# Kernel tuning notes

Measured on AMD Instinct MI355X. Metric: run time of the kernel, lower is better.

Reference implementation:

```python
import jax, jax.numpy as jnp
import numpy as np

B, K, E, D = 256, 2, 16, 512  # batch, top_k, num_experts, input_dim==output_dim
EPS = 1e-5  # nn.LayerNorm default eps
SCALE = 0.02  # param init scale


def setup_inputs() -> dict:
    key = jax.random.key(0)
    ks = jax.random.split(key, 9)
    return {
        "x": jax.random.normal(ks[0], (B, D), dtype=jnp.float32),
        "weight_probs": jax.random.uniform(ks[1], (B, K), dtype=jnp.float32),
        "bias_probs": jax.random.uniform(ks[2], (B, K), dtype=jnp.float32),
        "input_weight_bank": jax.random.normal(ks[3], (E, D, D), dtype=jnp.float32) * SCALE,
        "output_weight_bank": jax.random.normal(ks[4], (E, D, D), dtype=jnp.float32) * SCALE,
        "diagonal_weight_bank": jax.random.normal(ks[5], (E, D, D), dtype=jnp.float32) * SCALE,
        "bias_bank": jax.random.normal(ks[6], (E, D, D), dtype=jnp.float32) * SCALE,
        "weight_indices": jax.random.randint(ks[7], (B, K), 0, E),
        "bias_indices": jax.random.randint(ks[8], (B, K), 0, E),
    }


def reference(x, weight_probs, bias_probs, input_weight_bank, output_weight_bank,
              diagonal_weight_bank, bias_bank, weight_indices, bias_indices):
    # gather per-example expert parameter slabs: [B, K, D, D]
    iv = jnp.einsum('bi,bkij->bkj', x, input_weight_bank[weight_indices])     # [B,K,D]
    ov = jnp.einsum('bi,bkij->bkj', x, output_weight_bank[weight_indices])    # [B,K,D]
    dv = jnp.einsum('bi,bkij->bkj', x, diagonal_weight_bank[weight_indices])  # [B,K,D]

    # outer-product generated weight matrix + dynamic diagonal (in==out, no padding)
    outer = iv[..., :, None] * ov[..., None, :]                               # [B,K,D,D]
    r = jnp.arange(D)
    W = outer.at[..., r, r].add(dv)                                           # add diag embed

    # probability-weighted combine over top-k (weight_probs reshaped (-1,K,1,1) in torch)
    Wmix = jnp.einsum('bk,bkio->bio', weight_probs, W)                        # [B,D,D]

    # LayerNorm over output_dim, elementwise_affine=False
    mu = jnp.mean(Wmix, axis=-1, keepdims=True)
    var = jnp.var(Wmix, axis=-1, keepdims=True)
    Wn = (Wmix - mu) * jax.lax.rsqrt(var + EPS)

    # generated biases: gather + einsum + weighted combine ((-1,K,1) reshape)
    bv = jnp.einsum('bi,bkio->bko', x, bias_bank[bias_indices])               # [B,K,D]
    bmix = jnp.einsum('bk,bko->bo', bias_probs, bv)                           # [B,D]
    return (Wn, bmix)
```

## Files before the change

kernel.cpp:

```cpp
#include <hip/hip_runtime.h>
#include <math.h>

#define BB 256
#define KK 2
#define EE 16
#define DD 512
#define BK (BB*KK)
#define NP 4

#define WCH 18432
#define BCH 18560
#define WS_F_BASE 20480
#define SLAB (BK*DD)

__global__ void build_lists(const int* __restrict__ widx,
                            const int* __restrict__ bidx,
                            int* __restrict__ ws) {
    __shared__ int scw[16], scb[16];
    int* wlist = ws + 1024;
    int* blist = ws + 10240;
    const int t = threadIdx.x;
    if (t < 16) { scw[t] = 0; scb[t] = 0; }
    __syncthreads();
    int e = widx[t];
    int p = atomicAdd(&scw[e], 1);
    wlist[e * BK + p] = t;
    int eb = bidx[t];
    int pb = atomicAdd(&scb[eb], 1);
    blist[eb * BK + pb] = t;
    __syncthreads();
    if (t == 0) {
        int nc = 0;
        for (int e2 = 0; e2 < 16; ++e2) {
            int n = scw[e2];
            for (int r = 0; r < n; r += 16)
                ws[WCH + 1 + nc++] = e2 | (r << 8) | (min(16, n - r) << 20);
        }
        ws[WCH] = nc;
    }
    if (t == 64) {
        int nc = 0;
        for (int e2 = 0; e2 < 16; ++e2) {
            int n = scb[e2];
            for (int r = 0; r < n; r += 16)
                ws[BCH + 1 + nc++] = e2 | (r << 8) | (min(16, n - r) << 20);
        }
        ws[BCH] = nc;
    }
}

__launch_bounds__(256)
__global__ void expert_vm(const float* __restrict__ x,
                          const float* __restrict__ w_in,
                          const float* __restrict__ w_out,
                          const float* __restrict__ w_diag,
                          const float* __restrict__ w_bias,
                          const int* __restrict__ ws_i,
                          float* __restrict__ ws_f) {
    const int zp = blockIdx.z;
    const int z = zp >> 2, ip = zp & 3;
    const int* ch = ws_i + ((z < 3) ? WCH : BCH);
    const int slot = blockIdx.y;
    if (slot >= ch[0]) return;
    const int desc = ch[1 + slot];
    const int e = desc & 0xff, r0 = (desc >> 8) & 0xfff, rows = desc >> 20;
    const int* list = ws_i + ((z < 3) ? 1024 : 10240) + e * BK + r0;
    const int i0 = ip * 128;
    const float* W = (z == 0 ? w_in : z == 1 ? w_out : z == 2 ? w_diag : w_bias)
                     + (size_t)e * DD * DD + (size_t)i0 * DD;
    float* out = ws_f + WS_F_BASE + (size_t)zp * SLAB;

    __shared__ int plist[16];
    __shared__ float4 xs[128][4];
    const int t = threadIdx.x;
    if (t < 16) plist[t] = (t < rows) ? list[t] : -1;
    __syncthreads();
    #pragma unroll
    for (int k = 0; k < 2; ++k) {
        int idx = t + k * 256;
        int i = idx >> 2, q = idx & 3;
        int p0 = plist[q * 4 + 0], p1 = plist[q * 4 + 1];
        int p2 = plist[q * 4 + 2], p3 = plist[q * 4 + 3];
        float4 v;
        v.x = (p0 >= 0) ? x[(p0 >> 1) * DD + i0 + i] : 0.f;
        v.y = (p1 >= 0) ? x[(p1 >> 1) * DD + i0 + i] : 0.f;
        v.z = (p2 >= 0) ? x[(p2 >> 1) * DD + i0 + i] : 0.f;
        v.w = (p3 >= 0) ? x[(p3 >> 1) * DD + i0 + i] : 0.f;
        xs[i][q] = v;
    }
    __syncthreads();

    const int col = blockIdx.x * 256 + t;
    const float* Wc = W + col;
    float acc[16];
    #pragma unroll
    for (int r = 0; r < 16; ++r) acc[r] = 0.f;

    #pragma unroll 8
    for (int i = 0; i < 128; ++i) {
        float w = Wc[(size_t)i * DD];
        float4 xa = xs[i][0];
        float4 xb = xs[i][1];
        float4 xc = xs[i][2];
        float4 xd = xs[i][3];
        acc[0]  += xa.x * w; acc[1]  += xa.y * w; acc[2]  += xa.z * w; acc[3]  += xa.w * w;
        acc[4]  += xb.x * w; acc[5]  += xb.y * w; acc[6]  += xb.z * w; acc[7]  += xb.w * w;
        acc[8]  += xc.x * w; acc[9]  += xc.y * w; acc[10] += xc.z * w; acc[11] += xc.w * w;
        acc[12] += xd.x * w; acc[13] += xd.y * w; acc[14] += xd.z * w; acc[15] += xd.w * w;
    }
    #pragma unroll
    for (int r = 0; r < 16; ++r) {
        int p = plist[r];
        if (p >= 0) out[(size_t)p * DD + col] = acc[r];
    }
}

__launch_bounds__(256)
__global__ void gen_write(const float* __restrict__ ws_f,
                          const float* __restrict__ wp,
                          const float* __restrict__ bp,
                          float* __restrict__ outp,
                          float* __restrict__ outb) {
    const int b = blockIdx.y;
    const int chunk = blockIdx.x;
    const float* base = ws_f + WS_F_BASE;

    __shared__ float4 ov1v[128], ov2v[128];
    __shared__ float S[5], red[20];
    __shared__ float saf1[64], saf2[64], scm[64], scc[64];
    const int t = threadIdx.x;
    const float* ov1 = (const float*)ov1v;
    const float* ov2 = (const float*)ov2v;

    {
        const int tt = t & 127;
        const int row = b * 2 + (t >> 7);
        float sx = 0.f, sy = 0.f, sz = 0.f, sw = 0.f;
        #pragma unroll
        for (int pp = 0; pp < NP; ++pp) {
            const float4* q4 = (const float4*)(base + (size_t)(4 + pp) * SLAB
                                               + (size_t)row * DD);
            float4 v = q4[tt];
            sx += v.x; sy += v.y; sz += v.z; sw += v.w;
        }
        float4 s = make_float4(sx, sy, sz, sw);
        if (t < 128) ov1v[tt] = s; else ov2v[tt] = s;
    }
    __syncthreads();

    float v0a = ov1[t], v0b = ov1[t + 256], v1a = ov2[t], v1b = ov2[t + 256];
    float s[5];
    s[0] = v0a + v0b;
    s[1] = v1a + v1b;
    s[2] = v0a * v0a + v0b * v0b;
    s[3] = v0a * v1a + v0b * v1b;
    s[4] = v1a * v1a + v1b * v1b;
    #pragma unroll
    for (int off = 32; off; off >>= 1) {
        #pragma unroll
        for (int q = 0; q < 5; ++q) s[q] += __shfl_down(s[q], off);
    }
    const int lane = t & 63, wv = t >> 6;
    if (lane == 0) {
        #pragma unroll
        for (int q = 0; q < 5; ++q) red[wv * 5 + q] = s[q];
    }
    __syncthreads();
    if (t == 0) {
        #pragma unroll
        for (int q = 0; q < 5; ++q) S[q] = red[q] + red[5 + q] + red[10 + q] + red[15 + q];
    }
    __syncthreads();

    if (t < 64) {
        const float S1 = S[0], S2 = S[1], S11 = S[2], S12 = S[3], S22 = S[4];
        int i = chunk * 64 + t;
        float wp0 = wp[b * 2], wp1 = wp[b * 2 + 1];
        float iv1 = 0.f, iv2 = 0.f, dv1 = 0.f, dv2 = 0.f;
        #pragma unroll
        for (int pp = 0; pp < NP; ++pp) {
            const float* s0 = base + (size_t)(0 + pp) * SLAB;
            const float* s2 = base + (size_t)(8 + pp) * SLAB;
            iv1 += s0[(size_t)(b * 2 + 0) * DD + i];
            iv2 += s0[(size_t)(b * 2 + 1) * DD + i];
            dv1 += s2[(size_t)(b * 2 + 0) * DD + i];
            dv2 += s2[(size_t)(b * 2 + 1) * DD + i];
        }
        float a1 = wp0 * iv1;
        float a2 = wp1 * iv2;
        float dd = wp0 * dv1 + wp1 * dv2;
        float mu = (a1 * S1 + a2 * S2 + dd) * (1.0f / DD);
        float e2 = (a1 * a1 * S11 + 2.0f * a1 * a2 * S12 + a2 * a2 * S22
                    + 2.0f * (a1 * ov1[i] + a2 * ov2[i]) * dd + dd * dd) * (1.0f / DD);
        float var = e2 - mu * mu;
        float rs = rsqrtf(var + 1e-5f);
        saf1[t] = a1 * rs;
        saf2[t] = a2 * rs;
        scm[t]  = -mu * rs;
        scc[t]  = dd * rs;
    }
    __syncthreads();

    const int ci = t & 127, rh = t >> 7;
    const float4 o1 = ov1v[ci], o2 = ov2v[ci];
    const int jj = ci * 4;
    float* obase = outp + ((size_t)b * DD + chunk * 64) * DD;
    #pragma unroll 2
    for (int rr = 0; rr < 32; ++rr) {
        int r = rr * 2 + rh;
        int irow = chunk * 64 + r;
        float af1 = saf1[r], af2 = saf2[r], cm = scm[r], cc = scc[r];
        float4 w;
        w.x = fmaf(af1, o1.x, fmaf(af2, o2.x, cm));
        w.y = fmaf(af1, o1.y, fmaf(af2, o2.y, cm));
        w.z = fmaf(af1, o1.z, fmaf(af2, o2.z, cm));
        w.w = fmaf(af1, o1.w, fmaf(af2, o2.w, cm));
        int d = irow - jj;
        w.x += (d == 0) ? cc : 0.f;
        w.y += (d == 1) ? cc : 0.f;
        w.z += (d == 2) ? cc : 0.f;
        w.w += (d == 3) ? cc : 0.f;
        ((float4*)(obase + (size_t)r * DD))[ci] = w;
    }

    if (chunk == 0) {
        float p0 = bp[b * 2], p1 = bp[b * 2 + 1];
        float s0a = 0.f, s0b = 0.f, s1a = 0.f, s1b = 0.f;
        #pragma unroll
        for (int pp = 0; pp < NP; ++pp) {
            const float* bv = base + (size_t)(12 + pp) * SLAB;
            s0a += bv[(size_t)(b * 2 + 0) * DD + t];
            s0b += bv[(size_t)(b * 2 + 0) * DD + t + 256];
            s1a += bv[(size_t)(b * 2 + 1) * DD + t];
            s1b += bv[(size_t)(b * 2 + 1) * DD + t + 256];
        }
        outb[(size_t)b * DD + t]       = p0 * s0a + p1 * s1a;
        outb[(size_t)b * DD + t + 256] = p0 * s0b + p1 * s1b;
    }
}

extern "C" void kernel_launch(void* const* d_in, const int* in_sizes, int n_in,
                              void* d_out, int out_size, void* d_ws, size_t ws_size,
                              hipStream_t stream) {
    const float* x      = (const float*)d_in[0];
    const float* wprobs = (const float*)d_in[1];
    const float* bprobs = (const float*)d_in[2];
    const float* w_in   = (const float*)d_in[3];
    const float* w_out  = (const float*)d_in[4];
    const float* w_diag = (const float*)d_in[5];
    const float* w_bias = (const float*)d_in[6];
    const int*   widx   = (const int*)d_in[7];
    const int*   bidx   = (const int*)d_in[8];
    float* out = (float*)d_out;
    int*   wsI = (int*)d_ws;
    float* wsF = (float*)d_ws;

    build_lists<<<1, BK, 0, stream>>>(widx, bidx, wsI);

    expert_vm<<<dim3(2, 48, 16), 256, 0, stream>>>(x, w_in, w_out, w_diag, w_bias,
                                                   wsI, wsF);

    gen_write<<<dim3(8, BB), 256, 0, stream>>>(wsF, wprobs, bprobs, out,
                                               out + (size_t)BB * DD * DD);
}
```

Baseline: 393.4 us.

## Process 32 rows per expert chunk and stage weight tiles in shared memory

Expert row chunks grow from 16 to 32 rows, so each weight column load is reused across twice as many (batch, k) rows and fewer chunk blocks are launched. Weight tiles of 32x256 are loaded with coalesced float4 reads into shared memory before the FMA loop, replacing direct strided per-thread global loads. The cost is 32 accumulators per thread, which raises register pressure, plus extra LDS usage and synchronisation that may lower occupancy.

```diff
diff --git a/kernel.cpp b/kernel.cpp
--- a/kernel.cpp
+++ b/kernel.cpp
@@ -33,8 +33,8 @@
         int nc = 0;
         for (int e2 = 0; e2 < 16; ++e2) {
             int n = scw[e2];
-            for (int r = 0; r < n; r += 16)
-                ws[WCH + 1 + nc++] = e2 | (r << 8) | (min(16, n - r) << 20);
+            for (int r = 0; r < n; r += 32)
+                ws[WCH + 1 + nc++] = e2 | (r << 8) | (min(32, n - r) << 20);
         }
         ws[WCH] = nc;
     }
@@ -42,8 +42,8 @@
         int nc = 0;
         for (int e2 = 0; e2 < 16; ++e2) {
             int n = scb[e2];
-            for (int r = 0; r < n; r += 16)
-                ws[BCH + 1 + nc++] = e2 | (r << 8) | (min(16, n - r) << 20);
+            for (int r = 0; r < n; r += 32)
+                ws[BCH + 1 + nc++] = e2 | (r << 8) | (min(32, n - r) << 20);
         }
         ws[BCH] = nc;
     }
@@ -66,19 +66,21 @@
     const int e = desc & 0xff, r0 = (desc >> 8) & 0xfff, rows = desc >> 20;
     const int* list = ws_i + ((z < 3) ? 1024 : 10240) + e * BK + r0;
     const int i0 = ip * 128;
+    const int colbase = blockIdx.x * 256;
     const float* W = (z == 0 ? w_in : z == 1 ? w_out : z == 2 ? w_diag : w_bias)
-                     + (size_t)e * DD * DD + (size_t)i0 * DD;
+                     + (size_t)e * DD * DD + (size_t)i0 * DD + colbase;
     float* out = ws_f + WS_F_BASE + (size_t)zp * SLAB;
 
-    __shared__ int plist[16];
-    __shared__ float4 xs[128][4];
+    __shared__ int plist[32];
+    __shared__ float4 xs[128][8];
+    __shared__ float  Wt[32][256];
     const int t = threadIdx.x;
-    if (t < 16) plist[t] = (t < rows) ? list[t] : -1;
-    __syncthreads();
-    #pragma unroll
-    for (int k = 0; k < 2; ++k) {
+    if (t < 32) plist[t] = (t < rows) ? list[t] : -1;
+    __syncthreads();
+    #pragma unroll
+    for (int k = 0; k < 4; ++k) {
         int idx = t + k * 256;
-        int i = idx >> 2, q = idx & 3;
+        int i = idx >> 3, q = idx & 7;
         int p0 = plist[q * 4 + 0], p1 = plist[q * 4 + 1];
         int p2 = plist[q * 4 + 2], p3 = plist[q * 4 + 3];
         float4 v;
@@ -88,28 +90,39 @@
         v.w = (p3 >= 0) ? x[(p3 >> 1) * DD + i0 + i] : 0.f;
         xs[i][q] = v;
     }
-    __syncthreads();
-
-    const int col = blockIdx.x * 256 + t;
-    const float* Wc = W + col;
-    float acc[16];
-    #pragma unroll
-    for (int r = 0; r < 16; ++r) acc[r] = 0.f;
-
-    #pragma unroll 8
-    for (int i = 0; i < 128; ++i) {
-        float w = Wc[(size_t)i * DD];
-        float4 xa = xs[i][0];
-        float4 xb = xs[i][1];
-        float4 xc = xs[i][2];
-        float4 xd = xs[i][3];
-        acc[0]  += xa.x * w; acc[1]  += xa.y * w; acc[2]  += xa.z * w; acc[3]  += xa.w * w;
-        acc[4]  += xb.x * w; acc[5]  += xb.y * w; acc[6]  += xb.z * w; acc[7]  += xb.w * w;
-        acc[8]  += xc.x * w; acc[9]  += xc.y * w; acc[10] += xc.z * w; acc[11] += xc.w * w;
-        acc[12] += xd.x * w; acc[13] += xd.y * w; acc[14] += xd.z * w; acc[15] += xd.w * w;
-    }
-    #pragma unroll
-    for (int r = 0; r < 16; ++r) {
+
+    float acc[32];
+    #pragma unroll
+    for (int r = 0; r < 32; ++r) acc[r] = 0.f;
+
+    const int srow = t >> 6, sc4 = (t & 63);
+
+    for (int s = 0; s < 4; ++s) {
+        __syncthreads();
+        #pragma unroll
+        for (int j = 0; j < 8; ++j) {
+            int row = srow + j * 4;
+            float4 v = *(const float4*)(W + (size_t)(s * 32 + row) * DD + sc4 * 4);
+            *(float4*)&Wt[row][sc4 * 4] = v;
+        }
+        __syncthreads();
+        #pragma unroll 4
+        for (int ii = 0; ii < 32; ++ii) {
+            int i = s * 32 + ii;
+            float w = Wt[ii][t];
+            #pragma unroll
+            for (int q = 0; q < 8; ++q) {
+                float4 xv = xs[i][q];
+                acc[q * 4 + 0] += xv.x * w;
+                acc[q * 4 + 1] += xv.y * w;
+                acc[q * 4 + 2] += xv.z * w;
+                acc[q * 4 + 3] += xv.w * w;
+            }
+        }
+    }
+    const int col = colbase + t;
+    #pragma unroll
+    for (int r = 0; r < 32; ++r) {
         int p = plist[r];
         if (p >= 0) out[(size_t)p * DD + col] = acc[r];
     }
@@ -257,7 +270,7 @@
 
     build_lists<<<1, BK, 0, stream>>>(widx, bidx, wsI);
 
-    expert_vm<<<dim3(2, 48, 16), 256, 0, stream>>>(x, w_in, w_out, w_diag, w_bias,
+    expert_vm<<<dim3(2, 32, 16), 256, 0, stream>>>(x, w_in, w_out, w_diag, w_bias,
                                                    wsI, wsF);
 
     gen_write<<<dim3(8, BB), 256, 0, stream>>>(wsF, wprobs, bprobs, out,
```

Result: slower. 430.3 us (+9.4%).
